# Kernel optimization log

Hardware: AMD Instinct MI355X
Metric: run time of the kernel (lower is better)

## Reference

```python
import jax, jax.numpy as jnp
import numpy as np

N, D, H, C, L, G, E = 50000, 128, 128, 40, 3, 4, 800000
GRID = jnp.linspace(-2.0, 2.0, G)          # RBF grid on [-2, 2]
DENOM = 4.0 / (G - 1)                      # (grid_max - grid_min) / (num_grids - 1)


def _layernorm(x, g, b, eps=1e-5):
    m = x.mean(-1, keepdims=True)
    v = x.var(-1, keepdims=True)
    return (x - m) * jax.lax.rsqrt(v + eps) * g + b


def _fkan(x, ln_g, ln_b, sw, bw, bb):
    # FastKANLayer: layernorm -> Gaussian RBF basis -> bias-free spline linear, + silu base update
    xn = _layernorm(x, ln_g, ln_b)
    basis = jnp.exp(-(((xn[..., None] - GRID) / DENOM) ** 2))     # [n, d, G]
    ret = basis.reshape(x.shape[0], -1) @ sw.T                    # [n, out]
    return ret + jax.nn.silu(x) @ bw.T + bb


def _gcn_prop(h, src, dst, n):
    # symmetric GCN normalization with self-loops already appended to src/dst
    deg = jax.ops.segment_sum(jnp.ones(src.shape[0], h.dtype), dst, num_segments=n)
    dis = jnp.where(deg > 0, jax.lax.rsqrt(deg), 0.0)
    norm = dis[src] * dis[dst]                                    # [e]
    return jax.ops.segment_sum(h[src] * norm[:, None], dst, num_segments=n)


def _batchnorm(x, g, b, eps=1e-5):
    m = x.mean(0)
    v = x.var(0)  # biased variance, as torch BN uses for normalization
    return (x - m) * jax.lax.rsqrt(v + eps) * g + b


def setup_inputs() -> dict:
    key = jax.random.key(0)
    ks = jax.random.split(key, 8)
    x = jax.random.normal(ks[0], (N, D), jnp.float32)
    edge_index = jax.random.randint(ks[1], (2, E), 0, N, jnp.int64)
    return {
        "x": x,
        "edge_index": edge_index,
        "ln_g": jnp.ones((L, D), jnp.float32),
        "ln_b": jnp.zeros((L, D), jnp.float32),
        "sw": jax.random.normal(ks[2], (L, H, D * G), jnp.float32) * 0.1,
        "bw": jax.random.normal(ks[3], (L, H, D), jnp.float32) * (1.0 / np.sqrt(D)),
        "bb": jnp.zeros((L, H), jnp.float32),
        "gcn_bias": jnp.zeros((L, H), jnp.float32),
        "bn_g": jnp.ones((L, H), jnp.float32),
        "bn_b": jnp.zeros((L, H), jnp.float32),
        "ln_g_out": jnp.ones((D + L * H,), jnp.float32),
        "ln_b_out": jnp.zeros((D + L * H,), jnp.float32),
        "sw_out": jax.random.normal(ks[4], (C, (D + L * H) * G), jnp.float32) * 0.1,
        "bw_out": jax.random.normal(ks[5], (C, D + L * H), jnp.float32) * (1.0 / np.sqrt(D + L * H)),
        "bb_out": jnp.zeros((C,), jnp.float32),
    }


def reference(x, edge_index, ln_g, ln_b, sw, bw, bb, gcn_bias, bn_g, bn_b,
              ln_g_out, ln_b_out, sw_out, bw_out, bb_out):
    loops = jnp.arange(N, dtype=edge_index.dtype)
    src = jnp.concatenate([edge_index[0], loops])
    dst = jnp.concatenate([edge_index[1], loops])
    feats = [x]
    h = x
    for i in range(L):  # fixed small layer count
        h = _fkan(h, ln_g[i], ln_b[i], sw[i], bw[i], bb[i])
        h = _gcn_prop(h, src, dst, N) + gcn_bias[i]
        h = _batchnorm(h, bn_g[i], bn_b[i])
        feats.append(h)
    xcat = jnp.concatenate(feats, axis=1)  # [N, D + L*H] skip-concat
    return _fkan(xcat, ln_g_out, ln_b_out, sw_out, bw_out, bb_out)
```

## Files before the change

kernel.cpp:

```cpp
#include <hip/hip_runtime.h>
#include <hip/hip_bf16.h>

#define TPB 256
#define TPBO 512

typedef __attribute__((ext_vector_type(8))) short s8v;
typedef __attribute__((ext_vector_type(4))) float f32x4;
typedef unsigned short u16;

__device__ __forceinline__ u16 f2bf(float f){
  union { __hip_bfloat16 h; u16 u; } cv;
  cv.h = __float2bfloat16(f);
  return cv.u;
}

__device__ __forceinline__ unsigned pack_bf2(float lo, float hi){
  return (unsigned)f2bf(lo) | ((unsigned)f2bf(hi) << 16);
}

__device__ __forceinline__ float bflo(unsigned u){ return __uint_as_float(u << 16); }
__device__ __forceinline__ float bfhi(unsigned u){ return __uint_as_float(u & 0xffff0000u); }

__device__ __forceinline__ float wave_sum(float v){
  #pragma unroll
  for (int off=32; off>0; off>>=1) v += __shfl_xor(v, off, 64);
  return v;
}

__device__ __forceinline__ int wave_incl_scan(int v, int lane){
  #pragma unroll
  for (int off=1; off<64; off<<=1){
    int u = __shfl_up(v, off, 64);
    if (lane >= off) v += u;
  }
  return v;
}

__global__ __launch_bounds__(TPB) void count_k(const int* __restrict__ dstE, int* __restrict__ cnt, int E){
  int e = blockIdx.x*TPB + threadIdx.x;
  if (e < E) atomicAdd(&cnt[dstE[e]], 1);
}

__global__ __launch_bounds__(TPB) void dis_k(const int* __restrict__ cnt, float* __restrict__ disp, int nN){
  int n = blockIdx.x*TPB + threadIdx.x;
  if (n < nN) disp[n] = rsqrtf((float)cnt[n] + 1.0f);
}

__global__ __launch_bounds__(TPB) void scan1_k(const int* __restrict__ cnt, int* __restrict__ rowptr,
                                               int* __restrict__ bsum, int nN){
  int t = threadIdx.x;
  int i = blockIdx.x*TPB + t;
  int lane = t & 63, wid = t >> 6;
  int v = (i < nN) ? cnt[i] : 0;
  int inc = wave_incl_scan(v, lane);
  __shared__ int wsum[4];
  if (lane == 63) wsum[wid] = inc;
  __syncthreads();
  int off = 0;
  #pragma unroll
  for (int w=0; w<4; ++w) if (w < wid) off += wsum[w];
  if (i < nN) rowptr[i] = inc - v + off;
  if (t == 0) bsum[blockIdx.x] = wsum[0]+wsum[1]+wsum[2]+wsum[3];
}

__global__ __launch_bounds__(TPB) void scan2_k(int* __restrict__ bsum, int nbk){
  int t = threadIdx.x;
  int lane = t & 63, wid = t >> 6;
  int v = (t < nbk) ? bsum[t] : 0;
  int inc = wave_incl_scan(v, lane);
  __shared__ int wsum[4];
  if (lane == 63) wsum[wid] = inc;
  __syncthreads();
  int off = 0;
  #pragma unroll
  for (int w=0; w<4; ++w) if (w < wid) off += wsum[w];
  __syncthreads();
  if (t < nbk) bsum[t] = inc - v + off;
}

__global__ __launch_bounds__(TPB) void scan3_k(int* __restrict__ rowptr, const int* __restrict__ bsum, int nN, int E){
  int i = blockIdx.x*TPB + threadIdx.x;
  if (i < nN) rowptr[i] += bsum[blockIdx.x];
  if (i == 0) rowptr[nN] = E;
}

__global__ __launch_bounds__(TPB) void fill_k(const int* __restrict__ srcE, const int* __restrict__ dstE,
                                              const int* __restrict__ rowptr, int* __restrict__ cursor,
                                              int* __restrict__ csr, int E){
  int e = blockIdx.x*TPB + threadIdx.x;
  if (e >= E) return;
  int d = dstE[e];
  int pos = atomicAdd(&cursor[d], 1);
  csr[rowptr[d] + pos] = srcE[e];
}

__global__ __launch_bounds__(TPB) void ln512_k(const float* __restrict__ x, const u16* __restrict__ hl16,
                                               const float* __restrict__ scshAll,
                                               float* __restrict__ meanp, float* __restrict__ rstdp, int nN){
  int g = blockIdx.x*TPB + threadIdx.x;
  int n = g >> 6, lane = g & 63;
  if (n >= nN) return;
  float s = 0.f, sq = 0.f;
  #pragma unroll
  for (int k=0;k<8;k++){
    float v;
    if (k < 2){
      v = x[(size_t)n*128 + lane + k*64];
    } else {
      int k2 = k - 2, li = k2 >> 1, cc = lane + (k2&1)*64;
      float raw = __uint_as_float(((unsigned)hl16[((size_t)li*nN + n)*128 + cc]) << 16);
      v = fmaf(raw, scshAll[li*256 + cc], scshAll[li*256 + 128 + cc]);
    }
    s += v; sq += v*v;
  }
  s = wave_sum(s); sq = wave_sum(sq);
  float m = s * (1.f/512.f);
  float var = fmaxf(sq * (1.f/512.f) - m*m, 0.f);
  if (lane == 0){ meanp[n] = m; rstdp[n] = rsqrtf(var + 1e-5f); }
}

__global__ __launch_bounds__(TPB) void prep_wpre_k(const float* __restrict__ sw, const float* __restrict__ bw,
                                                   u16* __restrict__ wpre, int IN, int KSTEPS, int NTILES, int OUTW){
  int idx = blockIdx.x*TPB + threadIdx.x;
  if (idx >= NTILES*KSTEPS*512) return;
  int b = idx & 7, lane = (idx >> 3) & 63, rest = idx >> 9;
  int kstep = rest % KSTEPS, nt = rest / KSTEPS;
  int chunk = kstep / 5, g = kstep % 5;
  int d = chunk*32 + ((lane >> 4)*8 + b);
  int n = nt*16 + (lane & 15);
  float v = 0.f;
  if (n < OUTW) v = (g < 4) ? sw[(size_t)n*IN*4 + d*4 + g] : bw[(size_t)n*IN + d];
  wpre[idx] = f2bf(v);
}

__device__ __forceinline__ void build_frags(const float* __restrict__ h8, float mean, float rstd,
                                            const float* __restrict__ lngv, const float* __restrict__ lnbv,
                                            s8v* __restrict__ a){
  float bas[5][8];
  #pragma unroll
  for (int u=0; u<8; ++u){
    float v = h8[u];
    float xn = (v - mean)*rstd*lngv[u] + lnbv[u];
    float y = 0.900841806f*xn;
    float d0 = y + 1.80168361f;
    float d1 = y + 0.600561204f;
    float d2 = y - 0.600561204f;
    float d3 = y - 1.80168361f;
    bas[0][u] = __builtin_amdgcn_exp2f(-d0*d0);
    bas[1][u] = __builtin_amdgcn_exp2f(-d1*d1);
    bas[2][u] = __builtin_amdgcn_exp2f(-d2*d2);
    bas[3][u] = __builtin_amdgcn_exp2f(-d3*d3);
    float e = __builtin_amdgcn_exp2f(-1.44269504f*v);
    bas[4][u] = v * __builtin_amdgcn_rcpf(1.f + e);
  }
  #pragma unroll
  for (int g=0; g<5; ++g){
    #pragma unroll
    for (int j=0; j<4; ++j)
      ((unsigned*)&a[g])[j] = pack_bf2(bas[g][2*j], bas[g][2*j+1]);
  }
}

template<bool BF16IN>
__global__ __launch_bounds__(TPB) void fkan_layer_k(
    const float* __restrict__ in32, const u16* __restrict__ in16,
    const float* __restrict__ scsh,
    const float* __restrict__ lng, const float* __restrict__ lnb,
    const u16* __restrict__ wpre, const float* __restrict__ bias,
    const float* __restrict__ disp, u16* __restrict__ hs, int nN)
{
  const int t = threadIdx.x;
  const int wv = blockIdx.x*(TPB/64) + (t >> 6);
  const int ngrp = (nN + 15) >> 4;
  const int ng = wv >> 1, jh = wv & 1;
  if (ng >= ngrp) return;
  const int l = t & 63, clo = l & 15, kq = l >> 4;
  const int node = ng*16 + clo;
  const int nc = node < nN ? node : nN-1;

  float h[4][8];
  #pragma unroll
  for (int c=0; c<4; ++c){
    if (BF16IN){
      uint4 raw = *(const uint4*)(in16 + (size_t)nc*128 + c*32 + kq*8);
      h[c][0]=bflo(raw.x); h[c][1]=bfhi(raw.x);
      h[c][2]=bflo(raw.y); h[c][3]=bfhi(raw.y);
      h[c][4]=bflo(raw.z); h[c][5]=bfhi(raw.z);
      h[c][6]=bflo(raw.w); h[c][7]=bfhi(raw.w);
      #pragma unroll
      for (int u=0; u<8; ++u){
        int d = c*32 + kq*8 + u;
        h[c][u] = fmaf(h[c][u], scsh[d], scsh[128 + d]);
      }
    } else {
      const float* hrow = in32 + (size_t)nc*128;
      *(float4*)&h[c][0] = *(const float4*)(hrow + c*32 + kq*8);
      *(float4*)&h[c][4] = *(const float4*)(hrow + c*32 + kq*8 + 4);
    }
  }
  float s = 0.f, sq = 0.f;
  #pragma unroll
  for (int c=0; c<4; ++c)
    #pragma unroll
    for (int u=0; u<8; ++u){ float v = h[c][u]; s += v; sq += v*v; }
  s  += __shfl_xor(s, 16, 64);  s  += __shfl_xor(s, 32, 64);
  sq += __shfl_xor(sq, 16, 64); sq += __shfl_xor(sq, 32, 64);
  float mean = s * (1.f/128.f);
  float var  = fmaxf(sq * (1.f/128.f) - mean*mean, 0.f);
  float rstd = rsqrtf(var + 1e-5f);

  f32x4 acc[4];
  #pragma unroll
  for (int j=0; j<4; ++j) acc[j] = (f32x4)0.f;

  for (int c=0; c<4; ++c){
    float lngv[8], lnbv[8];
    *(float4*)&lngv[0] = *(const float4*)(lng + c*32 + kq*8);
    *(float4*)&lngv[4] = *(const float4*)(lng + c*32 + kq*8 + 4);
    *(float4*)&lnbv[0] = *(const float4*)(lnb + c*32 + kq*8);
    *(float4*)&lnbv[4] = *(const float4*)(lnb + c*32 + kq*8 + 4);
    s8v a[5];
    build_frags(h[c], mean, rstd, lngv, lnbv, a);
    #pragma unroll
    for (int ks=0; ks<5; ++ks){
      const int kglob = c*5 + ks;
      #pragma unroll
      for (int j=0; j<4; ++j){
        s8v b = *(const s8v*)(wpre + ((size_t)((jh*4 + j)*20 + kglob)*64 + l)*8);
        acc[j] = __builtin_amdgcn_mfma_f32_16x16x32_bf16(a[ks], b, acc[j], 0, 0, 0);
      }
    }
  }
  float bv[4];
  #pragma unroll
  for (int j=0; j<4; ++j) bv[j] = bias[(jh*4 + j)*16 + clo];
  #pragma unroll
  for (int rr=0; rr<4; ++rr){
    int nw = ng*16 + kq*4 + rr;
    if (nw < nN){
      float dsc = disp[nw];
      #pragma unroll
      for (int j=0; j<4; ++j)
        hs[(size_t)nw*128 + (jh*4 + j)*16 + clo] = f2bf((acc[j][rr] + bv[j]) * dsc);
    }
  }
}

__global__ __launch_bounds__(TPBO) void fkan_out_k(
    const float* __restrict__ x, const u16* __restrict__ hl16,
    const float* __restrict__ scshAll,
    const float* __restrict__ meanp, const float* __restrict__ rstdp,
    const float* __restrict__ lng, const float* __restrict__ lnb,
    const u16* __restrict__ wpre, const float* __restrict__ bias,
    float* __restrict__ out, int nN)
{
  __shared__ float sred[8][24][64];
  const int t = threadIdx.x;
  const int w = t >> 6, l = t & 63, clo = l & 15, kq = l >> 4;
  const int nb0 = blockIdx.x * 32;
  int nc0 = nb0 + clo;      nc0 = nc0 < nN ? nc0 : nN-1;
  int nc1 = nb0 + 16 + clo; nc1 = nc1 < nN ? nc1 : nN-1;
  const float mean0 = meanp[nc0], rstd0 = rstdp[nc0];
  const float mean1 = meanp[nc1], rstd1 = rstdp[nc1];

  f32x4 acc[2][3];
  #pragma unroll
  for (int m=0; m<2; ++m)
    #pragma unroll
    for (int j=0; j<3; ++j) acc[m][j] = (f32x4)0.f;

  #pragma unroll
  for (int cc=0; cc<2; ++cc){
    const int c = w*2 + cc;
    const int d0 = c*32 + kq*8;
    float lngv[8], lnbv[8];
    *(float4*)&lngv[0] = *(const float4*)(lng + d0);
    *(float4*)&lngv[4] = *(const float4*)(lng + d0 + 4);
    *(float4*)&lnbv[0] = *(const float4*)(lnb + d0);
    *(float4*)&lnbv[4] = *(const float4*)(lnb + d0 + 4);
    float h0[8], h1[8];
    if (d0 < 128){
      const float* s0 = x + (size_t)nc0*128 + d0;
      const float* s1 = x + (size_t)nc1*128 + d0;
      *(float4*)&h0[0] = *(const float4*)(s0);  *(float4*)&h0[4] = *(const float4*)(s0+4);
      *(float4*)&h1[0] = *(const float4*)(s1);  *(float4*)&h1[4] = *(const float4*)(s1+4);
    } else {
      int dd = d0 - 128, li = dd >> 7, cc2 = dd & 127;
      uint4 r0 = *(const uint4*)(hl16 + ((size_t)li*nN + nc0)*128 + cc2);
      uint4 r1 = *(const uint4*)(hl16 + ((size_t)li*nN + nc1)*128 + cc2);
      h0[0]=bflo(r0.x); h0[1]=bfhi(r0.x); h0[2]=bflo(r0.y); h0[3]=bfhi(r0.y);
      h0[4]=bflo(r0.z); h0[5]=bfhi(r0.z); h0[6]=bflo(r0.w); h0[7]=bfhi(r0.w);
      h1[0]=bflo(r1.x); h1[1]=bfhi(r1.x); h1[2]=bflo(r1.y); h1[3]=bfhi(r1.y);
      h1[4]=bflo(r1.z); h1[5]=bfhi(r1.z); h1[6]=bflo(r1.w); h1[7]=bfhi(r1.w);
      #pragma unroll
      for (int u=0; u<8; ++u){
        float sc = scshAll[li*256 + cc2 + u], sh = scshAll[li*256 + 128 + cc2 + u];
        h0[u] = fmaf(h0[u], sc, sh);
        h1[u] = fmaf(h1[u], sc, sh);
      }
    }
    s8v a0[5], a1[5];
    build_frags(h0, mean0, rstd0, lngv, lnbv, a0);
    build_frags(h1, mean1, rstd1, lngv, lnbv, a1);
    #pragma unroll
    for (int ks=0; ks<5; ++ks){
      const int kglob = c*5 + ks;
      #pragma unroll
      for (int j=0; j<3; ++j){
        s8v b = *(const s8v*)(wpre + ((size_t)(j*80 + kglob)*64 + l)*8);
        acc[0][j] = __builtin_amdgcn_mfma_f32_16x16x32_bf16(a0[ks], b, acc[0][j], 0, 0, 0);
        acc[1][j] = __builtin_amdgcn_mfma_f32_16x16x32_bf16(a1[ks], b, acc[1][j], 0, 0, 0);
      }
    }
  }
  #pragma unroll
  for (int m=0; m<2; ++m)
    #pragma unroll
    for (int j=0; j<3; ++j)
      #pragma unroll
      for (int rr=0; rr<4; ++rr)
        sred[w][m*12 + j*4 + rr][l] = acc[m][j][rr];
  __syncthreads();
  #pragma unroll
  for (int k=0; k<3; ++k){
    int q = t + k*TPBO;
    int slot = q >> 6, l2 = q & 63;
    float val = 0.f;
    #pragma unroll
    for (int ww=0; ww<8; ++ww) val += sred[ww][slot][l2];
    int m = slot >= 12 ? 1 : 0;
    int jrr = slot - m*12;
    int j = jrr >> 2, rr = jrr & 3;
    int nodeq = nb0 + m*16 + (l2 >> 4)*4 + rr;
    int col = j*16 + (l2 & 15);
    if (nodeq < nN && col < 40)
      out[(size_t)nodeq*40 + col] = val + bias[col];
  }
}

__device__ __forceinline__ void acc_bf8(uint4 u, float* __restrict__ a){
  a[0] += bflo(u.x); a[1] += bfhi(u.x);
  a[2] += bflo(u.y); a[3] += bfhi(u.y);
  a[4] += bflo(u.z); a[5] += bfhi(u.z);
  a[6] += bflo(u.w); a[7] += bfhi(u.w);
}

__global__ __launch_bounds__(TPB) void gcn_k(const u16* __restrict__ hs, const int* __restrict__ rowptr,
                                             const int* __restrict__ csr, const float* __restrict__ disp,
                                             u16* __restrict__ hl, int nN){
  int g = blockIdx.x*TPB + threadIdx.x;
  int n = g >> 6, lane = g & 63;
  if (n >= nN) return;
  const uint4* H4 = (const uint4*)hs;
  const int li = lane & 15, qd = lane >> 4;
  int e0 = rowptr[n], e1 = rowptr[n+1];
  float a[8];
  #pragma unroll
  for (int j=0; j<8; ++j) a[j] = 0.f;
  for (int base = e0; base < e1; base += 16){
    int r[4];
    #pragma unroll
    for (int k=0; k<4; ++k){
      int idx = base + qd*4 + k;
      int idc = idx < e1 ? idx : e1-1;
      int rv  = csr[idc];
      r[k] = idx < e1 ? rv : nN;
    }
    #pragma unroll
    for (int k=0; k<4; ++k){
      uint4 u = H4[(size_t)r[k]*16 + li];
      acc_bf8(u, a);
    }
  }
  #pragma unroll
  for (int j=0; j<8; ++j){
    a[j] += __shfl_xor(a[j], 16, 64);
    a[j] += __shfl_xor(a[j], 32, 64);
  }
  if (qd == 0){
    uint4 u = H4[(size_t)n*16 + li];
    acc_bf8(u, a);
    float dn = disp[n];
    uint4 o;
    o.x = pack_bf2(a[0]*dn, a[1]*dn);
    o.y = pack_bf2(a[2]*dn, a[3]*dn);
    o.z = pack_bf2(a[4]*dn, a[5]*dn);
    o.w = pack_bf2(a[6]*dn, a[7]*dn);
    *(uint4*)(hl + (size_t)n*128 + li*8) = o;
  }
}

__global__ __launch_bounds__(TPB) void bn_stat_k(const u16* __restrict__ hl, float* __restrict__ stats, int nN){
  int cp   = threadIdx.x & 63;
  int strm = threadIdx.x >> 6;
  const unsigned* H = (const unsigned*)hl;
  float s0=0.f, s1=0.f, q0=0.f, q1=0.f;
  for (int r = blockIdx.x*4 + strm; r < nN; r += gridDim.x*4){
    unsigned u = H[(size_t)r*64 + cp];
    float lo = bflo(u), hi = bfhi(u);
    s0 += lo; q0 += lo*lo; s1 += hi; q1 += hi*hi;
  }
  __shared__ float ls[4][64][4];
  ls[strm][cp][0] = s0; ls[strm][cp][1] = q0; ls[strm][cp][2] = s1; ls[strm][cp][3] = q1;
  __syncthreads();
  if (strm == 0){
    float S0 = ls[0][cp][0]+ls[1][cp][0]+ls[2][cp][0]+ls[3][cp][0];
    float Q0 = ls[0][cp][1]+ls[1][cp][1]+ls[2][cp][1]+ls[3][cp][1];
    float S1 = ls[0][cp][2]+ls[1][cp][2]+ls[2][cp][2]+ls[3][cp][2];
    float Q1 = ls[0][cp][3]+ls[1][cp][3]+ls[2][cp][3]+ls[3][cp][3];
    atomicAdd(&stats[cp*2],       S0);
    atomicAdd(&stats[cp*2+1],     S1);
    atomicAdd(&stats[128+cp*2],   Q0);
    atomicAdd(&stats[128+cp*2+1], Q1);
  }
}

__global__ void bn_fin_k(const float* __restrict__ stats, const float* __restrict__ g, const float* __restrict__ b,
                         float* __restrict__ scsh, int nN){
  int c = threadIdx.x;
  float inv = 1.f/(float)nN;
  float m = stats[c]*inv;
  float var = fmaxf(stats[128+c]*inv - m*m, 0.f);
  float sc = g[c]*rsqrtf(var + 1e-5f);
  scsh[c] = sc;
  scsh[128+c] = b[c] - m*sc;
}

extern "C" void kernel_launch(void* const* d_in, const int* in_sizes, int n_in,
                              void* d_out, int out_size, void* d_ws, size_t ws_size,
                              hipStream_t stream)
{
  const float* x        = (const float*)d_in[0];
  const int*   ei       = (const int*)d_in[1];
  const float* ln_g     = (const float*)d_in[2];
  const float* ln_b     = (const float*)d_in[3];
  const float* sw       = (const float*)d_in[4];
  const float* bw       = (const float*)d_in[5];
  const float* bb       = (const float*)d_in[6];
  const float* bn_g     = (const float*)d_in[8];
  const float* bn_b     = (const float*)d_in[9];
  const float* ln_g_out = (const float*)d_in[10];
  const float* ln_b_out = (const float*)d_in[11];
  const float* sw_out   = (const float*)d_in[12];
  const float* bw_out   = (const float*)d_in[13];
  const float* bb_out   = (const float*)d_in[14];
  float* out = (float*)d_out;

  const int nN = in_sizes[0] / 128;
  const int E  = in_sizes[1] / 2;

  char* ws = (char*)d_ws;
  size_t off = 0;
  auto alloc = [&](size_t bytes)->char*{
    char* p = ws + off; off = (off + bytes + 255) & ~size_t(255); return p;
  };
  u16*   hl16  = (u16*)alloc((size_t)3*nN*128*2);
  u16*   hs    = (u16*)alloc((size_t)(nN+1)*128*2);
  float* meanp = (float*)alloc((size_t)nN*4);
  float* rstdp = (float*)alloc((size_t)nN*4);
  float* disp  = (float*)alloc((size_t)nN*4);
  float* stats = (float*)alloc(256*4);
  float* scshL = (float*)alloc(3*256*4);
  u16*   wpreL = (u16*)alloc((size_t)3*8*20*512*2);
  u16*   wpreO = (u16*)alloc((size_t)3*80*512*2);
  int* cnt     = (int*)alloc((size_t)nN*4);
  int* cursor  = (int*)alloc((size_t)nN*4);
  int* rowptr  = (int*)alloc((size_t)(nN+1)*4);
  int* bsum    = (int*)alloc(256*4);
  int* csr     = (int*)alloc((size_t)E*4);
  (void)ws_size; (void)n_in; (void)out_size;

  const int* srcE = ei;
  const int* dstE = ei + E;

  hipMemsetAsync(cnt, 0, (size_t)nN*4, stream);
  hipMemsetAsync(cursor, 0, (size_t)nN*4, stream);
  hipMemsetAsync(hs + (size_t)nN*128, 0, 256, stream);

  for (int i=0; i<3; ++i)
    prep_wpre_k<<<(8*20*512 + TPB-1)/TPB, TPB, 0, stream>>>(
        sw + (size_t)i*128*512, bw + (size_t)i*128*128, wpreL + (size_t)i*8*20*512, 128, 20, 8, 128);
  prep_wpre_k<<<(3*80*512 + TPB-1)/TPB, TPB, 0, stream>>>(
      sw_out, bw_out, wpreO, 512, 80, 3, 40);

  const int nbE = (E + TPB-1)/TPB;
  const int nbN = (nN + TPB-1)/TPB;
  count_k<<<nbE, TPB, 0, stream>>>(dstE, cnt, E);
  dis_k<<<nbN, TPB, 0, stream>>>(cnt, disp, nN);
  scan1_k<<<nbN, TPB, 0, stream>>>(cnt, rowptr, bsum, nN);
  scan2_k<<<1, TPB, 0, stream>>>(bsum, nbN);
  scan3_k<<<nbN, TPB, 0, stream>>>(rowptr, bsum, nN, E);
  fill_k<<<nbE, TPB, 0, stream>>>(srcE, dstE, rowptr, cursor, csr, E);

  const int nbW = (nN*64 + TPB-1)/TPB;
  const int nbL = (((nN + 15)/16)*2 + 3)/4;
  const int nbO = (nN + 31)/32;

  for (int i=0; i<3; ++i){
    if (i == 0){
      fkan_layer_k<false><<<nbL, TPB, 0, stream>>>(
          x, (const u16*)nullptr, (const float*)nullptr,
          ln_g, ln_b, wpreL, bb, disp, hs, nN);
    } else {
      fkan_layer_k<true><<<nbL, TPB, 0, stream>>>(
          (const float*)nullptr, hl16 + (size_t)(i-1)*nN*128, scshL + (size_t)(i-1)*256,
          ln_g + (size_t)i*128, ln_b + (size_t)i*128,
          wpreL + (size_t)i*8*20*512, bb + (size_t)i*128, disp, hs, nN);
    }
    gcn_k<<<nbW, TPB, 0, stream>>>(hs, rowptr, csr, disp, hl16 + (size_t)i*nN*128, nN);
    hipMemsetAsync(stats, 0, 256*4, stream);
    bn_stat_k<<<256, TPB, 0, stream>>>(hl16 + (size_t)i*nN*128, stats, nN);
    bn_fin_k<<<1, 128, 0, stream>>>(stats, bn_g + (size_t)i*128, bn_b + (size_t)i*128,
                                    scshL + (size_t)i*256, nN);
  }

  ln512_k<<<nbW, TPB, 0, stream>>>(x, hl16, scshL, meanp, rstdp, nN);
  fkan_out_k<<<nbO, TPBO, 0, stream>>>(
      x, hl16, scshL, meanp, rstdp, ln_g_out, ln_b_out, wpreO, bb_out, out, nN);
}
```

Before: 438.4 us.

## Fuse output layernorm stats into fkan_out and fold dis into scan1

Removes the separate ln512 kernel by computing per-row mean/variance inside fkan_out_k. Each wave holds its 16-column slice of the 512-wide row in registers, reduces with shuffles, and combines the eight waves through shared memory. This avoids a second full read of x and hl16 and the meanp/rstdp round trip. The dis_k kernel is also folded into scan1_k, and a launch-bounds occupancy hint of 4 is added to fkan_out_k. The cost is higher register pressure, since the whole row slice is now kept live across the MFMA loop.

Result: no change. 434.8 us (-0.8%).

```diff
diff --git a/kernel.cpp b/kernel.cpp
--- a/kernel.cpp
+++ b/kernel.cpp
@@ -21,12 +21,6 @@
 __device__ __forceinline__ float bflo(unsigned u){ return __uint_as_float(u << 16); }
 __device__ __forceinline__ float bfhi(unsigned u){ return __uint_as_float(u & 0xffff0000u); }
 
-__device__ __forceinline__ float wave_sum(float v){
-  #pragma unroll
-  for (int off=32; off>0; off>>=1) v += __shfl_xor(v, off, 64);
-  return v;
-}
-
 __device__ __forceinline__ int wave_incl_scan(int v, int lane){
   #pragma unroll
   for (int off=1; off<64; off<<=1){
@@ -41,17 +35,13 @@
   if (e < E) atomicAdd(&cnt[dstE[e]], 1);
 }
 
-__global__ __launch_bounds__(TPB) void dis_k(const int* __restrict__ cnt, float* __restrict__ disp, int nN){
-  int n = blockIdx.x*TPB + threadIdx.x;
-  if (n < nN) disp[n] = rsqrtf((float)cnt[n] + 1.0f);
-}
-
 __global__ __launch_bounds__(TPB) void scan1_k(const int* __restrict__ cnt, int* __restrict__ rowptr,
-                                               int* __restrict__ bsum, int nN){
+                                               int* __restrict__ bsum, float* __restrict__ disp, int nN){
   int t = threadIdx.x;
   int i = blockIdx.x*TPB + t;
   int lane = t & 63, wid = t >> 6;
   int v = (i < nN) ? cnt[i] : 0;
+  if (i < nN) disp[i] = rsqrtf((float)v + 1.0f);
   int inc = wave_incl_scan(v, lane);
   __shared__ int wsum[4];
   if (lane == 63) wsum[wid] = inc;
@@ -92,31 +82,6 @@
   int d = dstE[e];
   int pos = atomicAdd(&cursor[d], 1);
   csr[rowptr[d] + pos] = srcE[e];
-}
-
-__global__ __launch_bounds__(TPB) void ln512_k(const float* __restrict__ x, const u16* __restrict__ hl16,
-                                               const float* __restrict__ scshAll,
-                                               float* __restrict__ meanp, float* __restrict__ rstdp, int nN){
-  int g = blockIdx.x*TPB + threadIdx.x;
-  int n = g >> 6, lane = g & 63;
-  if (n >= nN) return;
-  float s = 0.f, sq = 0.f;
-  #pragma unroll
-  for (int k=0;k<8;k++){
-    float v;
-    if (k < 2){
-      v = x[(size_t)n*128 + lane + k*64];
-    } else {
-      int k2 = k - 2, li = k2 >> 1, cc = lane + (k2&1)*64;
-      float raw = __uint_as_float(((unsigned)hl16[((size_t)li*nN + n)*128 + cc]) << 16);
-      v = fmaf(raw, scshAll[li*256 + cc], scshAll[li*256 + 128 + cc]);
-    }
-    s += v; sq += v*v;
-  }
-  s = wave_sum(s); sq = wave_sum(sq);
-  float m = s * (1.f/512.f);
-  float var = fmaxf(sq * (1.f/512.f) - m*m, 0.f);
-  if (lane == 0){ meanp[n] = m; rstdp[n] = rsqrtf(var + 1e-5f); }
 }
 
 __global__ __launch_bounds__(TPB) void prep_wpre_k(const float* __restrict__ sw, const float* __restrict__ bw,
@@ -246,22 +211,75 @@
   }
 }
 
-__global__ __launch_bounds__(TPBO) void fkan_out_k(
+__global__ __launch_bounds__(TPBO, 4) void fkan_out_k(
     const float* __restrict__ x, const u16* __restrict__ hl16,
     const float* __restrict__ scshAll,
-    const float* __restrict__ meanp, const float* __restrict__ rstdp,
     const float* __restrict__ lng, const float* __restrict__ lnb,
     const u16* __restrict__ wpre, const float* __restrict__ bias,
     float* __restrict__ out, int nN)
 {
+  __shared__ float sstat[8][16][4];
   __shared__ float sred[8][24][64];
   const int t = threadIdx.x;
   const int w = t >> 6, l = t & 63, clo = l & 15, kq = l >> 4;
   const int nb0 = blockIdx.x * 32;
   int nc0 = nb0 + clo;      nc0 = nc0 < nN ? nc0 : nN-1;
   int nc1 = nb0 + 16 + clo; nc1 = nc1 < nN ? nc1 : nN-1;
-  const float mean0 = meanp[nc0], rstd0 = rstdp[nc0];
-  const float mean1 = meanp[nc1], rstd1 = rstdp[nc1];
+
+  float h0[2][8], h1[2][8];
+  #pragma unroll
+  for (int cc=0; cc<2; ++cc){
+    const int c = w*2 + cc;
+    const int d0 = c*32 + kq*8;
+    if (d0 < 128){
+      const float* s0 = x + (size_t)nc0*128 + d0;
+      const float* s1 = x + (size_t)nc1*128 + d0;
+      *(float4*)&h0[cc][0] = *(const float4*)(s0);  *(float4*)&h0[cc][4] = *(const float4*)(s0+4);
+      *(float4*)&h1[cc][0] = *(const float4*)(s1);  *(float4*)&h1[cc][4] = *(const float4*)(s1+4);
+    } else {
+      int dd = d0 - 128, li = dd >> 7, cc2 = dd & 127;
+      uint4 r0 = *(const uint4*)(hl16 + ((size_t)li*nN + nc0)*128 + cc2);
+      uint4 r1 = *(const uint4*)(hl16 + ((size_t)li*nN + nc1)*128 + cc2);
+      h0[cc][0]=bflo(r0.x); h0[cc][1]=bfhi(r0.x); h0[cc][2]=bflo(r0.y); h0[cc][3]=bfhi(r0.y);
+      h0[cc][4]=bflo(r0.z); h0[cc][5]=bfhi(r0.z); h0[cc][6]=bflo(r0.w); h0[cc][7]=bfhi(r0.w);
+      h1[cc][0]=bflo(r1.x); h1[cc][1]=bfhi(r1.x); h1[cc][2]=bflo(r1.y); h1[cc][3]=bfhi(r1.y);
+      h1[cc][4]=bflo(r1.z); h1[cc][5]=bfhi(r1.z); h1[cc][6]=bflo(r1.w); h1[cc][7]=bfhi(r1.w);
+      #pragma unroll
+      for (int u=0; u<8; ++u){
+        float sc = scshAll[li*256 + cc2 + u], sh = scshAll[li*256 + 128 + cc2 + u];
+        h0[cc][u] = fmaf(h0[cc][u], sc, sh);
+        h1[cc][u] = fmaf(h1[cc][u], sc, sh);
+      }
+    }
+  }
+  float s0=0.f, q0=0.f, s1=0.f, q1=0.f;
+  #pragma unroll
+  for (int cc=0; cc<2; ++cc)
+    #pragma unroll
+    for (int u=0; u<8; ++u){
+      float a0v = h0[cc][u], a1v = h1[cc][u];
+      s0 += a0v; q0 += a0v*a0v;
+      s1 += a1v; q1 += a1v*a1v;
+    }
+  s0 += __shfl_xor(s0, 16, 64); s0 += __shfl_xor(s0, 32, 64);
+  q0 += __shfl_xor(q0, 16, 64); q0 += __shfl_xor(q0, 32, 64);
+  s1 += __shfl_xor(s1, 16, 64); s1 += __shfl_xor(s1, 32, 64);
+  q1 += __shfl_xor(q1, 16, 64); q1 += __shfl_xor(q1, 32, 64);
+  if (l < 16){
+    sstat[w][clo][0] = s0; sstat[w][clo][1] = q0;
+    sstat[w][clo][2] = s1; sstat[w][clo][3] = q1;
+  }
+  __syncthreads();
+  float S0=0.f, Q0=0.f, S1=0.f, Q1=0.f;
+  #pragma unroll
+  for (int ww=0; ww<8; ++ww){
+    S0 += sstat[ww][clo][0]; Q0 += sstat[ww][clo][1];
+    S1 += sstat[ww][clo][2]; Q1 += sstat[ww][clo][3];
+  }
+  const float mean0 = S0 * (1.f/512.f);
+  const float rstd0 = rsqrtf(fmaxf(Q0*(1.f/512.f) - mean0*mean0, 0.f) + 1e-5f);
+  const float mean1 = S1 * (1.f/512.f);
+  const float rstd1 = rsqrtf(fmaxf(Q1*(1.f/512.f) - mean1*mean1, 0.f) + 1e-5f);
 
   f32x4 acc[2][3];
   #pragma unroll
@@ -278,30 +296,9 @@
     *(float4*)&lngv[4] = *(const float4*)(lng + d0 + 4);
     *(float4*)&lnbv[0] = *(const float4*)(lnb + d0);
     *(float4*)&lnbv[4] = *(const float4*)(lnb + d0 + 4);
-    float h0[8], h1[8];
-    if (d0 < 128){
-      const float* s0 = x + (size_t)nc0*128 + d0;
-      const float* s1 = x + (size_t)nc1*128 + d0;
-      *(float4*)&h0[0] = *(const float4*)(s0);  *(float4*)&h0[4] = *(const float4*)(s0+4);
-      *(float4*)&h1[0] = *(const float4*)(s1);  *(float4*)&h1[4] = *(const float4*)(s1+4);
-    } else {
-      int dd = d0 - 128, li = dd >> 7, cc2 = dd & 127;
-      uint4 r0 = *(const uint4*)(hl16 + ((size_t)li*nN + nc0)*128 + cc2);
-      uint4 r1 = *(const uint4*)(hl16 + ((size_t)li*nN + nc1)*128 + cc2);
-      h0[0]=bflo(r0.x); h0[1]=bfhi(r0.x); h0[2]=bflo(r0.y); h0[3]=bfhi(r0.y);
-      h0[4]=bflo(r0.z); h0[5]=bfhi(r0.z); h0[6]=bflo(r0.w); h0[7]=bfhi(r0.w);
-      h1[0]=bflo(r1.x); h1[1]=bfhi(r1.x); h1[2]=bflo(r1.y); h1[3]=bfhi(r1.y);
-      h1[4]=bflo(r1.z); h1[5]=bfhi(r1.z); h1[6]=bflo(r1.w); h1[7]=bfhi(r1.w);
-      #pragma unroll
-      for (int u=0; u<8; ++u){
-        float sc = scshAll[li*256 + cc2 + u], sh = scshAll[li*256 + 128 + cc2 + u];
-        h0[u] = fmaf(h0[u], sc, sh);
-        h1[u] = fmaf(h1[u], sc, sh);
-      }
-    }
     s8v a0[5], a1[5];
-    build_frags(h0, mean0, rstd0, lngv, lnbv, a0);
-    build_frags(h1, mean1, rstd1, lngv, lnbv, a1);
+    build_frags(h0[cc], mean0, rstd0, lngv, lnbv, a0);
+    build_frags(h1[cc], mean1, rstd1, lngv, lnbv, a1);
     #pragma unroll
     for (int ks=0; ks<5; ++ks){
       const int kglob = c*5 + ks;
@@ -456,8 +453,6 @@
   };
   u16*   hl16  = (u16*)alloc((size_t)3*nN*128*2);
   u16*   hs    = (u16*)alloc((size_t)(nN+1)*128*2);
-  float* meanp = (float*)alloc((size_t)nN*4);
-  float* rstdp = (float*)alloc((size_t)nN*4);
   float* disp  = (float*)alloc((size_t)nN*4);
   float* stats = (float*)alloc(256*4);
   float* scshL = (float*)alloc(3*256*4);
@@ -486,8 +481,7 @@
   const int nbE = (E + TPB-1)/TPB;
   const int nbN = (nN + TPB-1)/TPB;
   count_k<<<nbE, TPB, 0, stream>>>(dstE, cnt, E);
-  dis_k<<<nbN, TPB, 0, stream>>>(cnt, disp, nN);
-  scan1_k<<<nbN, TPB, 0, stream>>>(cnt, rowptr, bsum, nN);
+  scan1_k<<<nbN, TPB, 0, stream>>>(cnt, rowptr, bsum, disp, nN);
   scan2_k<<<1, TPB, 0, stream>>>(bsum, nbN);
   scan3_k<<<nbN, TPB, 0, stream>>>(rowptr, bsum, nN, E);
   fill_k<<<nbE, TPB, 0, stream>>>(srcE, dstE, rowptr, cursor, csr, E);
@@ -514,7 +508,6 @@
                                     scshL + (size_t)i*256, nN);
   }
 
-  ln512_k<<<nbW, TPB, 0, stream>>>(x, hl16, scshL, meanp, rstdp, nN);
   fkan_out_k<<<nbO, TPBO, 0, stream>>>(
-      x, hl16, scshL, meanp, rstdp, ln_g_out, ln_b_out, wpreO, bb_out, out, nN);
-}
+      x, hl16, scshL, ln_g_out, ln_b_out, wpreO, bb_out, out, nN);
+}
```
